# Kernel tuning notes

Measured on AMD Instinct MI355X. Metric: run time of the kernel, lower is better.

Reference implementation:

```python
import jax, jax.numpy as jnp
import numpy as np

EXPANSION_RATES = [10, 25]
NEG_SLOPE = 0.2


def gat_layer(x_self, x_neigh, W, a_self, a_neigh):
    """Multi-head GAT attention over a fixed neighbor fanout.

    x_self:  [M, F]      target-node features
    x_neigh: [M, K, F]   K sampled neighbors per target
    W:       [H, F, D]   per-head projection
    a_self:  [H, D]      attention vector (self part)
    a_neigh: [H, D]      attention vector (neighbor part)
    returns  [M, H*D]    concatenated heads
    """
    hs = jnp.einsum('mf,hfd->mhd', x_self, W)              # [M,H,D]
    hn = jnp.einsum('mkf,hfd->mkhd', x_neigh, W)           # [M,K,H,D]
    e_self = jnp.einsum('mhd,hd->mh', hs, a_self)          # [M,H]
    e_neigh = jnp.einsum('mkhd,hd->mkh', hn, a_neigh)      # [M,K,H]
    e = jax.nn.leaky_relu(e_self[:, None, :] + e_neigh, NEG_SLOPE)
    alpha = jax.nn.softmax(e, axis=1)                      # softmax over K neighbors
    out = jnp.einsum('mkh,mkhd->mhd', alpha, hn)           # [M,H,D]
    return out.reshape(out.shape[0], -1)                   # concat heads


def setup_inputs() -> dict:
    key = jax.random.key(0)
    ks = jax.random.split(key, 10)
    B, F, D, H, OUT = 1024, 128, 128, 2, 128
    r0, r1 = EXPANSION_RATES
    inp = {}
    # hierarchical embeddings: level j has B * prod(rates[:j]) rows
    inp['h0'] = jax.random.normal(ks[0], (B, F), dtype=jnp.float32)
    inp['h1'] = jax.random.normal(ks[1], (B * r0, F), dtype=jnp.float32)
    inp['h2'] = jax.random.normal(ks[2], (B * r0 * r1, F), dtype=jnp.float32)
    # layer 0: consumes raw features (F); layer 1: consumes H*D
    inp['W0'] = jax.random.normal(ks[3], (H, F, D), dtype=jnp.float32) / np.sqrt(F)
    inp['a_self0'] = jax.random.normal(ks[4], (H, D), dtype=jnp.float32) / np.sqrt(D)
    inp['a_neigh0'] = jax.random.normal(ks[5], (H, D), dtype=jnp.float32) / np.sqrt(D)
    inp['W1'] = jax.random.normal(ks[6], (H, H * D, D), dtype=jnp.float32) / np.sqrt(H * D)
    inp['a_self1'] = jax.random.normal(ks[7], (H, D), dtype=jnp.float32) / np.sqrt(D)
    inp['a_neigh1'] = jax.random.normal(ks[8], (H, D), dtype=jnp.float32) / np.sqrt(D)
    inp['fc_W'] = jax.random.normal(ks[9], (H * D, OUT), dtype=jnp.float32) / np.sqrt(H * D)
    return inp


def reference(h0, h1, h2, W0, a_self0, a_neigh0, W1, a_self1, a_neigh1, fc_W):
    hidden = [h0, h1, h2]
    layers = [(W0, a_self0, a_neigh0), (W1, a_self1, a_neigh1)]
    depth = len(EXPANSION_RATES)
    for i, (W, a_s, a_n) in enumerate(layers):
        for j in range(depth - i):
            x_self = hidden[j]                                   # [M, F_i]
            M = x_self.shape[0]
            # neighbor rows of level j+1 grouped in blocks of expansion_rates[j]
            x_neigh = hidden[j + 1].reshape(M, EXPANSION_RATES[j], x_self.shape[1])
            hidden[j] = gat_layer(x_self, x_neigh, W, a_s, a_n)  # [M, H*D]
    return hidden[0] @ fc_W                                      # [B, OUT]
```

## Files before the change

kernel.cpp:

```cpp
#include <hip/hip_runtime.h>

#define LRELU_SLOPE 0.2f

#define OFF_UV0  0u
#define OFF_U1   512u
#define OFF_V1   1024u
#define OFF_P    1536u
#define OFF_PP   2048u
#define OFF_Q    4096u
#define OFF_R    69632u
#define OFF_Y1   135168u
#define OFF_Y0   2756608u

__device__ __forceinline__ float dot4(float4 a, float4 b) {
    return a.x * b.x + a.y * b.y + a.z * b.z + a.w * b.w;
}

__global__ __launch_bounds__(256)
void prepA_kernel(const float* __restrict__ W0, const float* __restrict__ as0,
                  const float* __restrict__ an0,
                  const float* __restrict__ W1, const float* __restrict__ as1,
                  const float* __restrict__ an1,
                  const float* __restrict__ fcW, float* __restrict__ ws) {
    __shared__ float s[32 * 129];
    const int b = blockIdx.x;
    const int t = threadIdx.x;
    if (b < 192) {
        const int wid = b * 4 + (t >> 6);
        const int lane = t & 63;
        const float *wrow, *as, *an;
        if (wid < 256) {
            wrow = W0 + (size_t)wid * 128;
            int h = wid >> 7;
            as = as0 + h * 128; an = an0 + h * 128;
        } else {
            int g = wid - 256;
            wrow = W1 + (size_t)g * 128;
            int h = g >> 8;
            as = as1 + h * 128; an = an1 + h * 128;
        }
        float2 w = *(const float2*)(wrow + 2 * lane);
        float2 sv = *(const float2*)(as + 2 * lane);
        float2 nv = *(const float2*)(an + 2 * lane);
        float au = w.x * sv.x + w.y * sv.y;
        float av = w.x * nv.x + w.y * nv.y;
        #pragma unroll
        for (int off = 32; off > 0; off >>= 1) {
            au += __shfl_xor(au, off);
            av += __shfl_xor(av, off);
        }
        if (lane == 0) {
            if (wid < 256) { ws[OFF_UV0 + wid] = au; ws[OFF_UV0 + 256 + wid] = av; }
            else { int g = wid - 256; ws[OFF_U1 + g] = au; ws[OFF_V1 + g] = av; }
        }
    } else {
        const int idx = b - 192;
        const int h = idx >> 3, g0 = (idx & 7) * 32;
        const float* Wh = W1 + (size_t)h * 32768;
        for (int ii = t * 4; ii < 32 * 128; ii += 1024) {
            int i = ii >> 7, d = ii & 127;
            float4 g4 = *(const float4*)(Wh + (size_t)(g0 + i) * 128 + d);
            s[i * 129 + d + 0] = g4.x;
            s[i * 129 + d + 1] = g4.y;
            s[i * 129 + d + 2] = g4.z;
            s[i * 129 + d + 3] = g4.w;
        }
        __syncthreads();
        const int dg = t & 31, rg = t >> 5;
        float4 acc[4];
        #pragma unroll
        for (int j = 0; j < 4; ++j) acc[j] = make_float4(0.f, 0.f, 0.f, 0.f);
        const float* fp = fcW + (size_t)h * 16384 + 4 * dg;
        #pragma unroll 4
        for (int d2 = 0; d2 < 128; ++d2) {
            float4 f4 = *(const float4*)(fp + (size_t)d2 * 128);
            #pragma unroll
            for (int j = 0; j < 4; ++j) {
                float x = s[(rg * 4 + j) * 129 + d2];
                acc[j].x += x * f4.x; acc[j].y += x * f4.y;
                acc[j].z += x * f4.z; acc[j].w += x * f4.w;
            }
        }
        float* Qp = ws + OFF_Q + (size_t)h * 32768;
        #pragma unroll
        for (int j = 0; j < 4; ++j)
            *(float4*)(Qp + (size_t)(g0 + rg * 4 + j) * 128 + 4 * dg) = acc[j];
    }
}

__global__ __launch_bounds__(256)
void big2_kernel(const float* __restrict__ h0, const float* __restrict__ h1,
                 const float* __restrict__ h2, const float* __restrict__ W0,
                 float* __restrict__ ws) {
    const int b = blockIdx.x;
    const int t = threadIdx.x;
    const float* uv0 = ws + OFF_UV0;

    if (b < 2560) {
        const int lane = t & 63;
        const int half = lane >> 5;
        const int fl = lane & 31;
        const int m = b * 4 + (t >> 6);
        const float* xnp = h2 + (size_t)m * 3200;
        const float* xsp = h1 + (size_t)m * 128;
        const float4 u0 = *(const float4*)(uv0 + 0 + 4 * fl);
        const float4 u1 = *(const float4*)(uv0 + 128 + 4 * fl);
        const float4 v0 = *(const float4*)(uv0 + 256 + 4 * fl);
        const float4 v1 = *(const float4*)(uv0 + 384 + 4 * fl);

        float4 xr[13];
        {
            const float* sp = half ? xsp : (xnp + 24 * 128);
            xr[0] = *(const float4*)(sp + 4 * fl);
        }
        #pragma unroll
        for (int i = 1; i < 13; ++i)
            xr[i] = *(const float4*)(xnp + (size_t)(2 * (i - 1) + half) * 128 + 4 * fl);

        float z0[13], z1[13];
        #pragma unroll
        for (int i = 0; i < 13; ++i) {
            bool selfrow = (i == 0) && half;
            float p0 = dot4(xr[i], selfrow ? u0 : v0);
            float p1 = dot4(xr[i], selfrow ? u1 : v1);
            #pragma unroll
            for (int off = 16; off > 0; off >>= 1) {
                p0 += __shfl_xor(p0, off);
                p1 += __shfl_xor(p1, off);
            }
            z0[i] = p0; z1[i] = p1;
        }
        const float es0 = __shfl(z0[0], 32);
        const float es1 = __shfl(z1[0], 32);
        float mx0 = -1e30f, mx1 = -1e30f;
        #pragma unroll
        for (int i = 0; i < 13; ++i) {
            if (i == 0 && half) { z0[i] = -1e30f; z1[i] = -1e30f; }
            else {
                float a = es0 + z0[i]; a = (a >= 0.f) ? a : LRELU_SLOPE * a;
                float c = es1 + z1[i]; c = (c >= 0.f) ? c : LRELU_SLOPE * c;
                z0[i] = a; z1[i] = c;
                mx0 = fmaxf(mx0, a); mx1 = fmaxf(mx1, c);
            }
        }
        mx0 = fmaxf(mx0, __shfl_xor(mx0, 32));
        mx1 = fmaxf(mx1, __shfl_xor(mx1, 32));
        float s0 = 0.f, s1 = 0.f;
        float4 A0 = make_float4(0.f, 0.f, 0.f, 0.f);
        float4 A1 = make_float4(0.f, 0.f, 0.f, 0.f);
        #pragma unroll
        for (int i = 0; i < 13; ++i) {
            float e0 = __expf(z0[i] - mx0);
            float e1 = __expf(z1[i] - mx1);
            s0 += e0; s1 += e1;
            A0.x += e0 * xr[i].x; A0.y += e0 * xr[i].y;
            A0.z += e0 * xr[i].z; A0.w += e0 * xr[i].w;
            A1.x += e1 * xr[i].x; A1.y += e1 * xr[i].y;
            A1.z += e1 * xr[i].z; A1.w += e1 * xr[i].w;
        }
        s0 += __shfl_xor(s0, 32); s1 += __shfl_xor(s1, 32);
        A0.x += __shfl_xor(A0.x, 32); A0.y += __shfl_xor(A0.y, 32);
        A0.z += __shfl_xor(A0.z, 32); A0.w += __shfl_xor(A0.w, 32);
        A1.x += __shfl_xor(A1.x, 32); A1.y += __shfl_xor(A1.y, 32);
        A1.z += __shfl_xor(A1.z, 32); A1.w += __shfl_xor(A1.w, 32);
        const float inv = 1.f / (half ? s1 : s0);
        const float4 S = half ? A1 : A0;
        float4 o;
        o.x = S.x * inv; o.y = S.y * inv; o.z = S.z * inv; o.w = S.w * inv;
        *(float4*)(ws + OFF_Y1 + (size_t)m * 256 + half * 128 + 4 * fl) = o;
    } else if (b < 2816) {
        const int lane = t & 63;
        const int half = lane >> 5;
        const int fl = lane & 31;
        const int m = (b - 2560) * 4 + (t >> 6);
        const float* xnp = h1 + (size_t)m * 1280;
        const float* xsp = h0 + (size_t)m * 128;
        const float4 u0 = *(const float4*)(uv0 + 0 + 4 * fl);
        const float4 u1 = *(const float4*)(uv0 + 128 + 4 * fl);
        const float4 v0 = *(const float4*)(uv0 + 256 + 4 * fl);
        const float4 v1 = *(const float4*)(uv0 + 384 + 4 * fl);

        float4 xr[6];
        xr[0] = *(const float4*)(xsp + 4 * fl);
        #pragma unroll
        for (int i = 1; i < 6; ++i)
            xr[i] = *(const float4*)(xnp + (size_t)(2 * (i - 1) + half) * 128 + 4 * fl);

        float z0[6], z1[6];
        #pragma unroll
        for (int i = 0; i < 6; ++i) {
            float p0 = dot4(xr[i], (i == 0) ? u0 : v0);
            float p1 = dot4(xr[i], (i == 0) ? u1 : v1);
            #pragma unroll
            for (int off = 16; off > 0; off >>= 1) {
                p0 += __shfl_xor(p0, off);
                p1 += __shfl_xor(p1, off);
            }
            z0[i] = p0; z1[i] = p1;
        }
        const float es0 = z0[0];
        const float es1 = z1[0];
        float mx0 = -1e30f, mx1 = -1e30f;
        #pragma unroll
        for (int i = 0; i < 6; ++i) {
            if (i == 0) { z0[i] = -1e30f; z1[i] = -1e30f; }
            else {
                float a = es0 + z0[i]; a = (a >= 0.f) ? a : LRELU_SLOPE * a;
                float c = es1 + z1[i]; c = (c >= 0.f) ? c : LRELU_SLOPE * c;
                z0[i] = a; z1[i] = c;
                mx0 = fmaxf(mx0, a); mx1 = fmaxf(mx1, c);
            }
        }
        mx0 = fmaxf(mx0, __shfl_xor(mx0, 32));
        mx1 = fmaxf(mx1, __shfl_xor(mx1, 32));
        float s0 = 0.f, s1 = 0.f;
        float4 A0 = make_float4(0.f, 0.f, 0.f, 0.f);
        float4 A1 = make_float4(0.f, 0.f, 0.f, 0.f);
        #pragma unroll
        for (int i = 0; i < 6; ++i) {
            float e0 = __expf(z0[i] - mx0);
            float e1 = __expf(z1[i] - mx1);
            s0 += e0; s1 += e1;
            A0.x += e0 * xr[i].x; A0.y += e0 * xr[i].y;
            A0.z += e0 * xr[i].z; A0.w += e0 * xr[i].w;
            A1.x += e1 * xr[i].x; A1.y += e1 * xr[i].y;
            A1.z += e1 * xr[i].z; A1.w += e1 * xr[i].w;
        }
        s0 += __shfl_xor(s0, 32); s1 += __shfl_xor(s1, 32);
        A0.x += __shfl_xor(A0.x, 32); A0.y += __shfl_xor(A0.y, 32);
        A0.z += __shfl_xor(A0.z, 32); A0.w += __shfl_xor(A0.w, 32);
        A1.x += __shfl_xor(A1.x, 32); A1.y += __shfl_xor(A1.y, 32);
        A1.z += __shfl_xor(A1.z, 32); A1.w += __shfl_xor(A1.w, 32);
        const float inv = 1.f / (half ? s1 : s0);
        const float4 S = half ? A1 : A0;
        float4 o;
        o.x = S.x * inv; o.y = S.y * inv; o.z = S.z * inv; o.w = S.w * inv;
        *(float4*)(ws + OFF_Y0 + (size_t)m * 256 + half * 128 + 4 * fl) = o;
    } else if (b < 2944) {
        const int wid = (b - 2816) * 4 + (t >> 6);
        const int lane = t & 63;
        const int h = wid >> 8, rest = wid & 255;
        const int h0i = rest >> 7;
        const float* wrow = W0 + (size_t)rest * 128;
        float2 w2 = *(const float2*)(wrow + 2 * lane);
        float2 su = *(const float2*)(ws + OFF_U1 + h * 256 + h0i * 128 + 2 * lane);
        float2 sv = *(const float2*)(ws + OFF_V1 + h * 256 + h0i * 128 + 2 * lane);
        float pu = w2.x * su.x + w2.y * su.y;
        float pv = w2.x * sv.x + w2.y * sv.y;
        #pragma unroll
        for (int off = 32; off > 0; off >>= 1) {
            pu += __shfl_xor(pu, off);
            pv += __shfl_xor(pv, off);
        }
        if (lane == 0) { ws[OFF_PP + wid] = pu; ws[OFF_P + wid] = pv; }
    } else {
        __shared__ float smem[4160];
        const int idx = b - 2944;
        const int h = idx >> 3;
        const int h0i = (idx >> 2) & 1;
        const int f0 = (idx & 3) * 32;
        const float* W0h = W0 + (size_t)h0i * 16384;
        for (int ii = t * 4; ii < 32 * 128; ii += 1024) {
            int i = ii >> 7, d = ii & 127;
            float4 g4 = *(const float4*)(W0h + (size_t)(f0 + i) * 128 + d);
            smem[i * 129 + d + 0] = g4.x;
            smem[i * 129 + d + 1] = g4.y;
            smem[i * 129 + d + 2] = g4.z;
            smem[i * 129 + d + 3] = g4.w;
        }
        __syncthreads();
        const int dg = t & 31, rg = t >> 5;
        float4 acc[4];
        #pragma unroll
        for (int j = 0; j < 4; ++j) acc[j] = make_float4(0.f, 0.f, 0.f, 0.f);
        const float* Qp = ws + OFF_Q + (size_t)h * 32768 + (size_t)h0i * 16384 + 4 * dg;
        #pragma unroll 4
        for (int d = 0; d < 128; ++d) {
            float4 q4 = *(const float4*)(Qp + (size_t)d * 128);
            #pragma unroll
            for (int j = 0; j < 4; ++j) {
                float x = smem[(rg * 4 + j) * 129 + d];
                acc[j].x += x * q4.x; acc[j].y += x * q4.y;
                acc[j].z += x * q4.z; acc[j].w += x * q4.w;
            }
        }
        float* Rp = ws + OFF_R + (size_t)h * 32768 + (size_t)h0i * 16384;
        #pragma unroll
        for (int j = 0; j < 4; ++j)
            *(float4*)(Rp + (size_t)(f0 + rg * 4 + j) * 128 + 4 * dg) = acc[j];
    }
}

__global__ __launch_bounds__(256)
void final_kernel(const float* __restrict__ ws, float* __restrict__ out) {
    __shared__ float xn[22 * 256];
    __shared__ float yb[1024];
    __shared__ float pr[2][2][128];
    __shared__ float en[2][11][2];
    __shared__ float al[2][10][2];
    const int t = threadIdx.x;
    const int m0 = blockIdx.x * 2;
    const int rlane = t & 63;
    const int rg = t >> 6;
    const float* P  = ws + OFF_P;
    const float* Pp = ws + OFF_PP;
    const float* Y1 = ws + OFF_Y1;
    const float* Y0 = ws + OFF_Y0;
    const float4 su0 = *(const float4*)(Pp + 0 + 4 * rlane);
    const float4 su1 = *(const float4*)(Pp + 256 + 4 * rlane);
    const float4 nv0 = *(const float4*)(P + 0 + 4 * rlane);
    const float4 nv1 = *(const float4*)(P + 256 + 4 * rlane);
    float4 g[6];
    #pragma unroll
    for (int i = 0; i < 6; ++i) {
        int rho = rg + 4 * i;
        if (rho < 22) {
            int r = rho / 11, k = rho % 11;
            int m = m0 + r;
            const float* src = (k < 10) ? (Y1 + ((size_t)m * 10 + k) * 256)
                                        : (Y0 + (size_t)m * 256);
            g[i] = *(const float4*)(src + 4 * rlane);
        }
    }
    #pragma unroll
    for (int i = 0; i < 6; ++i) {
        int rho = rg + 4 * i;
        if (rho < 22) {
            int r = rho / 11, k = rho % 11;
            *(float4*)(&xn[rho * 256 + 4 * rlane]) = g[i];
            float p0 = dot4(g[i], (k < 10) ? nv0 : su0);
            float p1 = dot4(g[i], (k < 10) ? nv1 : su1);
            #pragma unroll
            for (int off = 32; off > 0; off >>= 1) {
                p0 += __shfl_xor(p0, off);
                p1 += __shfl_xor(p1, off);
            }
            if (rlane == 0) { en[r][k][0] = p0; en[r][k][1] = p1; }
        }
    }
    __syncthreads();
    if (t < 128) {
        int r = t >> 6, h = (t >> 5) & 1, k = t & 31;
        float e = -1e30f;
        if (k < 10) {
            float z = en[r][10][h] + en[r][k][h];
            e = (z >= 0.f) ? z : LRELU_SLOPE * z;
        }
        float mx = e;
        #pragma unroll
        for (int off = 16; off > 0; off >>= 1) mx = fmaxf(mx, __shfl_xor(mx, off));
        float ex = (k < 10) ? __expf(e - mx) : 0.f;
        float sm = ex;
        #pragma unroll
        for (int off = 16; off > 0; off >>= 1) sm += __shfl_xor(sm, off);
        if (k < 10) al[r][k][h] = ex / sm;
    }
    __syncthreads();
    #pragma unroll
    for (int i = 0; i < 4; ++i) {
        int c = t + 256 * i;
        int r = c >> 9, rem = c & 511, h = rem >> 8, f = rem & 255;
        float acc = 0.f;
        #pragma unroll
        for (int k = 0; k < 10; ++k) acc += al[r][k][h] * xn[(r * 11 + k) * 256 + f];
        yb[c] = acc;
    }
    __syncthreads();
    {
        const int seg = t >> 7;
        const int o = t & 127;
        const float* Rv = ws + OFF_R + (size_t)seg * 256 * 128 + o;
        const float* y0p = yb + seg * 256;
        const float* y1p = yb + 512 + seg * 256;
        float a0 = 0.f, a1 = 0.f;
        #pragma unroll 8
        for (int gi = 0; gi < 256; ++gi) {
            float rv = Rv[(size_t)gi * 128];
            a0 += y0p[gi] * rv;
            a1 += y1p[gi] * rv;
        }
        pr[seg][0][o] = a0;
        pr[seg][1][o] = a1;
    }
    __syncthreads();
    {
        const int r = t >> 7, o = t & 127;
        out[(size_t)(m0 + r) * 128 + o] = pr[0][r][o] + pr[1][r][o];
    }
}

extern "C" void kernel_launch(void* const* d_in, const int* in_sizes, int n_in,
                              void* d_out, int out_size, void* d_ws, size_t ws_size,
                              hipStream_t stream) {
    const float* h0  = (const float*)d_in[0];
    const float* h1  = (const float*)d_in[1];
    const float* h2  = (const float*)d_in[2];
    const float* W0  = (const float*)d_in[3];
    const float* as0 = (const float*)d_in[4];
    const float* an0 = (const float*)d_in[5];
    const float* W1  = (const float*)d_in[6];
    const float* as1 = (const float*)d_in[7];
    const float* an1 = (const float*)d_in[8];
    const float* fcW = (const float*)d_in[9];
    float* outp = (float*)d_out;
    float* ws = (float*)d_ws;

    hipLaunchKernelGGL(prepA_kernel, dim3(208), dim3(256), 0, stream,
                       W0, as0, an0, W1, as1, an1, fcW, ws);
    hipLaunchKernelGGL(big2_kernel, dim3(2960), dim3(256), 0, stream,
                       h0, h1, h2, W0, ws);
    hipLaunchKernelGGL(final_kernel, dim3(512), dim3(256), 0, stream,
                       ws, outp);
}
```

Before: 66.87 us.

## Use online softmax with streamed neighbor loads and DPP reductions in big kernel

Swaps the register-resident all-neighbors-then-softmax scheme in the big layer-0 kernel for an online softmax. Neighbor rows are streamed in pairs with one-step prefetch, which cuts the live register set and may raise occupancy. Warp reductions now use DPP row operations for the intra-16-lane steps in place of the full shuffle ladders. The trade is extra exp and rescale work per step, a less parallel dependency chain, and fewer loads in flight per wave.

```diff
diff --git a/kernel.cpp b/kernel.cpp
--- a/kernel.cpp
+++ b/kernel.cpp
@@ -14,6 +14,30 @@
 
 __device__ __forceinline__ float dot4(float4 a, float4 b) {
     return a.x * b.x + a.y * b.y + a.z * b.z + a.w * b.w;
+}
+
+template<int CTRL>
+__device__ __forceinline__ float dppmov(float x) {
+    return __int_as_float(__builtin_amdgcn_update_dpp(
+        0, __float_as_int(x), CTRL, 0xf, 0xf, true));
+}
+__device__ __forceinline__ float sum16(float x) {
+    x += dppmov<0xB1>(x);
+    x += dppmov<0x4E>(x);
+    x += dppmov<0x141>(x);
+    x += dppmov<0x140>(x);
+    return x;
+}
+__device__ __forceinline__ float sum32(float x) {
+    x = sum16(x);
+    return x + __shfl_xor(x, 16);
+}
+__device__ __forceinline__ float sum64(float x) {
+    float y = sum32(x);
+    return y + __shfl_xor(y, 32);
+}
+__device__ __forceinline__ float lrelu(float x) {
+    return (x >= 0.f) ? x : LRELU_SLOPE * x;
 }
 
 __global__ __launch_bounds__(256)
@@ -42,13 +66,8 @@
         float2 w = *(const float2*)(wrow + 2 * lane);
         float2 sv = *(const float2*)(as + 2 * lane);
         float2 nv = *(const float2*)(an + 2 * lane);
-        float au = w.x * sv.x + w.y * sv.y;
-        float av = w.x * nv.x + w.y * nv.y;
-        #pragma unroll
-        for (int off = 32; off > 0; off >>= 1) {
-            au += __shfl_xor(au, off);
-            av += __shfl_xor(av, off);
-        }
+        float au = sum64(w.x * sv.x + w.y * sv.y);
+        float av = sum64(w.x * nv.x + w.y * nv.y);
         if (lane == 0) {
             if (wid < 256) { ws[OFF_UV0 + wid] = au; ws[OFF_UV0 + 256 + wid] = av; }
             else { int g = wid - 256; ws[OFF_U1 + g] = au; ws[OFF_V1 + g] = av; }
@@ -88,8 +107,35 @@
     }
 }
 
+__device__ __forceinline__ void upd2(float& m, float& s, float4& A,
+                                     float ea, float eb,
+                                     const float4& xa, const float4& xb) {
+    float mn = fmaxf(m, fmaxf(ea, eb));
+    float sc = __expf(m - mn);
+    float pa = __expf(ea - mn);
+    float pb = __expf(eb - mn);
+    s = s * sc + pa + pb;
+    A.x = A.x * sc + pa * xa.x + pb * xb.x;
+    A.y = A.y * sc + pa * xa.y + pb * xb.y;
+    A.z = A.z * sc + pa * xa.z + pb * xb.z;
+    A.w = A.w * sc + pa * xa.w + pb * xb.w;
+    m = mn;
+}
+__device__ __forceinline__ void upd1(float& m, float& s, float4& A,
+                                     float ea, const float4& xa) {
+    float mn = fmaxf(m, ea);
+    float sc = __expf(m - mn);
+    float pa = __expf(ea - mn);
+    s = s * sc + pa;
+    A.x = A.x * sc + pa * xa.x;
+    A.y = A.y * sc + pa * xa.y;
+    A.z = A.z * sc + pa * xa.z;
+    A.w = A.w * sc + pa * xa.w;
+    m = mn;
+}
+
 __global__ __launch_bounds__(256)
-void big2_kernel(const float* __restrict__ h0, const float* __restrict__ h1,
+void big3_kernel(const float* __restrict__ h0, const float* __restrict__ h1,
                  const float* __restrict__ h2, const float* __restrict__ W0,
                  float* __restrict__ ws) {
     const int b = blockIdx.x;
@@ -108,56 +154,46 @@
         const float4 v0 = *(const float4*)(uv0 + 256 + 4 * fl);
         const float4 v1 = *(const float4*)(uv0 + 384 + 4 * fl);
 
-        float4 xr[13];
-        {
-            const float* sp = half ? xsp : (xnp + 24 * 128);
-            xr[0] = *(const float4*)(sp + 4 * fl);
-        }
-        #pragma unroll
-        for (int i = 1; i < 13; ++i)
-            xr[i] = *(const float4*)(xnp + (size_t)(2 * (i - 1) + half) * 128 + 4 * fl);
-
-        float z0[13], z1[13];
-        #pragma unroll
-        for (int i = 0; i < 13; ++i) {
-            bool selfrow = (i == 0) && half;
-            float p0 = dot4(xr[i], selfrow ? u0 : v0);
-            float p1 = dot4(xr[i], selfrow ? u1 : v1);
-            #pragma unroll
-            for (int off = 16; off > 0; off >>= 1) {
-                p0 += __shfl_xor(p0, off);
-                p1 += __shfl_xor(p1, off);
-            }
-            z0[i] = p0; z1[i] = p1;
-        }
-        const float es0 = __shfl(z0[0], 32);
-        const float es1 = __shfl(z1[0], 32);
-        float mx0 = -1e30f, mx1 = -1e30f;
-        #pragma unroll
-        for (int i = 0; i < 13; ++i) {
-            if (i == 0 && half) { z0[i] = -1e30f; z1[i] = -1e30f; }
-            else {
-                float a = es0 + z0[i]; a = (a >= 0.f) ? a : LRELU_SLOPE * a;
-                float c = es1 + z1[i]; c = (c >= 0.f) ? c : LRELU_SLOPE * c;
-                z0[i] = a; z1[i] = c;
-                mx0 = fmaxf(mx0, a); mx1 = fmaxf(mx1, c);
-            }
-        }
-        mx0 = fmaxf(mx0, __shfl_xor(mx0, 32));
-        mx1 = fmaxf(mx1, __shfl_xor(mx1, 32));
-        float s0 = 0.f, s1 = 0.f;
+        float4 xs = *(const float4*)(xsp + 4 * fl);
+        const float es0 = sum32(dot4(xs, u0));
+        const float es1 = sum32(dot4(xs, u1));
+
+        float4 xa = *(const float4*)(xnp + (size_t)(0 + half) * 128 + 4 * fl);
+        float4 xb = *(const float4*)(xnp + (size_t)(2 + half) * 128 + 4 * fl);
+        float m0 = -1e30f, m1 = -1e30f, s0 = 0.f, s1 = 0.f;
         float4 A0 = make_float4(0.f, 0.f, 0.f, 0.f);
         float4 A1 = make_float4(0.f, 0.f, 0.f, 0.f);
         #pragma unroll
-        for (int i = 0; i < 13; ++i) {
-            float e0 = __expf(z0[i] - mx0);
-            float e1 = __expf(z1[i] - mx1);
-            s0 += e0; s1 += e1;
-            A0.x += e0 * xr[i].x; A0.y += e0 * xr[i].y;
-            A0.z += e0 * xr[i].z; A0.w += e0 * xr[i].w;
-            A1.x += e1 * xr[i].x; A1.y += e1 * xr[i].y;
-            A1.z += e1 * xr[i].z; A1.w += e1 * xr[i].w;
-        }
+        for (int c = 0; c < 6; ++c) {
+            float4 na, nb;
+            if (c < 5) {
+                na = *(const float4*)(xnp + (size_t)(4 * c + 4 + half) * 128 + 4 * fl);
+                nb = *(const float4*)(xnp + (size_t)(4 * c + 6 + half) * 128 + 4 * fl);
+            } else {
+                na = *(const float4*)(xnp + (size_t)24 * 128 + 4 * fl);
+                nb = na;
+            }
+            float ea0 = lrelu(es0 + sum32(dot4(xa, v0)));
+            float ea1 = lrelu(es1 + sum32(dot4(xa, v1)));
+            float eb0 = lrelu(es0 + sum32(dot4(xb, v0)));
+            float eb1 = lrelu(es1 + sum32(dot4(xb, v1)));
+            upd2(m0, s0, A0, ea0, eb0, xa, xb);
+            upd2(m1, s1, A1, ea1, eb1, xa, xb);
+            xa = na; xb = nb;
+        }
+        {
+            float e0 = lrelu(es0 + sum32(dot4(xa, v0)));
+            float e1 = lrelu(es1 + sum32(dot4(xa, v1)));
+            if (half) { e0 = -1e30f; e1 = -1e30f; }
+            upd1(m0, s0, A0, e0, xa);
+            upd1(m1, s1, A1, e1, xa);
+        }
+        float g0 = fmaxf(m0, __shfl_xor(m0, 32));
+        float g1 = fmaxf(m1, __shfl_xor(m1, 32));
+        float c0 = __expf(m0 - g0), c1 = __expf(m1 - g1);
+        s0 *= c0; s1 *= c1;
+        A0.x *= c0; A0.y *= c0; A0.z *= c0; A0.w *= c0;
+        A1.x *= c1; A1.y *= c1; A1.z *= c1; A1.w *= c1;
         s0 += __shfl_xor(s0, 32); s1 += __shfl_xor(s1, 32);
         A0.x += __shfl_xor(A0.x, 32); A0.y += __shfl_xor(A0.y, 32);
         A0.z += __shfl_xor(A0.z, 32); A0.w += __shfl_xor(A0.w, 32);
@@ -180,52 +216,45 @@
         const float4 v0 = *(const float4*)(uv0 + 256 + 4 * fl);
         const float4 v1 = *(const float4*)(uv0 + 384 + 4 * fl);
 
-        float4 xr[6];
-        xr[0] = *(const float4*)(xsp + 4 * fl);
-        #pragma unroll
-        for (int i = 1; i < 6; ++i)
-            xr[i] = *(const float4*)(xnp + (size_t)(2 * (i - 1) + half) * 128 + 4 * fl);
-
-        float z0[6], z1[6];
-        #pragma unroll
-        for (int i = 0; i < 6; ++i) {
-            float p0 = dot4(xr[i], (i == 0) ? u0 : v0);
-            float p1 = dot4(xr[i], (i == 0) ? u1 : v1);
-            #pragma unroll
-            for (int off = 16; off > 0; off >>= 1) {
-                p0 += __shfl_xor(p0, off);
-                p1 += __shfl_xor(p1, off);
-            }
-            z0[i] = p0; z1[i] = p1;
-        }
-        const float es0 = z0[0];
-        const float es1 = z1[0];
-        float mx0 = -1e30f, mx1 = -1e30f;
-        #pragma unroll
-        for (int i = 0; i < 6; ++i) {
-            if (i == 0) { z0[i] = -1e30f; z1[i] = -1e30f; }
-            else {
-                float a = es0 + z0[i]; a = (a >= 0.f) ? a : LRELU_SLOPE * a;
-                float c = es1 + z1[i]; c = (c >= 0.f) ? c : LRELU_SLOPE * c;
-                z0[i] = a; z1[i] = c;
-                mx0 = fmaxf(mx0, a); mx1 = fmaxf(mx1, c);
-            }
-        }
-        mx0 = fmaxf(mx0, __shfl_xor(mx0, 32));
-        mx1 = fmaxf(mx1, __shfl_xor(mx1, 32));
-        float s0 = 0.f, s1 = 0.f;
+        float4 xs = *(const float4*)(xsp + 4 * fl);
+        const float es0 = sum32(dot4(xs, u0));
+        const float es1 = sum32(dot4(xs, u1));
+
+        float4 xa = *(const float4*)(xnp + (size_t)(0 + half) * 128 + 4 * fl);
+        float4 xb = *(const float4*)(xnp + (size_t)(2 + half) * 128 + 4 * fl);
+        float m0 = -1e30f, m1 = -1e30f, s0 = 0.f, s1 = 0.f;
         float4 A0 = make_float4(0.f, 0.f, 0.f, 0.f);
         float4 A1 = make_float4(0.f, 0.f, 0.f, 0.f);
         #pragma unroll
-        for (int i = 0; i < 6; ++i) {
-            float e0 = __expf(z0[i] - mx0);
-            float e1 = __expf(z1[i] - mx1);
-            s0 += e0; s1 += e1;
-            A0.x += e0 * xr[i].x; A0.y += e0 * xr[i].y;
-            A0.z += e0 * xr[i].z; A0.w += e0 * xr[i].w;
-            A1.x += e1 * xr[i].x; A1.y += e1 * xr[i].y;
-            A1.z += e1 * xr[i].z; A1.w += e1 * xr[i].w;
-        }
+        for (int c = 0; c < 2; ++c) {
+            float4 na, nb;
+            if (c < 1) {
+                na = *(const float4*)(xnp + (size_t)(4 + half) * 128 + 4 * fl);
+                nb = *(const float4*)(xnp + (size_t)(6 + half) * 128 + 4 * fl);
+            } else {
+                na = *(const float4*)(xnp + (size_t)(8 + half) * 128 + 4 * fl);
+                nb = na;
+            }
+            float ea0 = lrelu(es0 + sum32(dot4(xa, v0)));
+            float ea1 = lrelu(es1 + sum32(dot4(xa, v1)));
+            float eb0 = lrelu(es0 + sum32(dot4(xb, v0)));
+            float eb1 = lrelu(es1 + sum32(dot4(xb, v1)));
+            upd2(m0, s0, A0, ea0, eb0, xa, xb);
+            upd2(m1, s1, A1, ea1, eb1, xa, xb);
+            xa = na; xb = nb;
+        }
+        {
+            float e0 = lrelu(es0 + sum32(dot4(xa, v0)));
+            float e1 = lrelu(es1 + sum32(dot4(xa, v1)));
+            upd1(m0, s0, A0, e0, xa);
+            upd1(m1, s1, A1, e1, xa);
+        }
+        float g0 = fmaxf(m0, __shfl_xor(m0, 32));
+        float g1 = fmaxf(m1, __shfl_xor(m1, 32));
+        float c0 = __expf(m0 - g0), c1 = __expf(m1 - g1);
+        s0 *= c0; s1 *= c1;
+        A0.x *= c0; A0.y *= c0; A0.z *= c0; A0.w *= c0;
+        A1.x *= c1; A1.y *= c1; A1.z *= c1; A1.w *= c1;
         s0 += __shfl_xor(s0, 32); s1 += __shfl_xor(s1, 32);
         A0.x += __shfl_xor(A0.x, 32); A0.y += __shfl_xor(A0.y, 32);
         A0.z += __shfl_xor(A0.z, 32); A0.w += __shfl_xor(A0.w, 32);
@@ -245,13 +274,8 @@
         float2 w2 = *(const float2*)(wrow + 2 * lane);
         float2 su = *(const float2*)(ws + OFF_U1 + h * 256 + h0i * 128 + 2 * lane);
         float2 sv = *(const float2*)(ws + OFF_V1 + h * 256 + h0i * 128 + 2 * lane);
-        float pu = w2.x * su.x + w2.y * su.y;
-        float pv = w2.x * sv.x + w2.y * sv.y;
-        #pragma unroll
-        for (int off = 32; off > 0; off >>= 1) {
-            pu += __shfl_xor(pu, off);
-            pv += __shfl_xor(pv, off);
-        }
+        float pu = sum64(w2.x * su.x + w2.y * su.y);
+        float pv = sum64(w2.x * sv.x + w2.y * sv.y);
         if (lane == 0) { ws[OFF_PP + wid] = pu; ws[OFF_P + wid] = pv; }
     } else {
         __shared__ float smem[4160];
@@ -328,13 +352,8 @@
         if (rho < 22) {
             int r = rho / 11, k = rho % 11;
             *(float4*)(&xn[rho * 256 + 4 * rlane]) = g[i];
-            float p0 = dot4(g[i], (k < 10) ? nv0 : su0);
-            float p1 = dot4(g[i], (k < 10) ? nv1 : su1);
-            #pragma unroll
-            for (int off = 32; off > 0; off >>= 1) {
-                p0 += __shfl_xor(p0, off);
-                p1 += __shfl_xor(p1, off);
-            }
+            float p0 = sum64(dot4(g[i], (k < 10) ? nv0 : su0));
+            float p1 = sum64(dot4(g[i], (k < 10) ? nv1 : su1));
             if (rlane == 0) { en[r][k][0] = p0; en[r][k][1] = p1; }
         }
     }
@@ -407,7 +426,7 @@
 
     hipLaunchKernelGGL(prepA_kernel, dim3(208), dim3(256), 0, stream,
                        W0, as0, an0, W1, as1, an1, fcW, ws);
-    hipLaunchKernelGGL(big2_kernel, dim3(2960), dim3(256), 0, stream,
+    hipLaunchKernelGGL(big3_kernel, dim3(2960), dim3(256), 0, stream,
                        h0, h1, h2, W0, ws);
     hipLaunchKernelGGL(final_kernel, dim3(512), dim3(256), 0, stream,
                        ws, outp);
```

After: 67.61 us. No clear change (+1.1%).
